# Optimization experiments

Measured on AMD Instinct MI355X. Metric: run time of the kernel, lower is better.

Reference implementation:

```python
import jax, jax.numpy as jnp
import numpy as np

B, H, C, HID, WIN, K = 8, 64, 128, 512, 4, 3
L = H * H

def _conv(x, w, groups, pad):
    return jax.lax.conv_general_dilated(
        x, w, (1, 1), [(pad, pad), (pad, pad)],
        dimension_numbers=('NCHW', 'OIHW', 'NCHW'), feature_group_count=groups)

def _ln(x, g, b):
    m = x.mean(-1, keepdims=True)
    v = ((x - m) ** 2).mean(-1, keepdims=True)
    return (x - m) * jax.lax.rsqrt(v + 1e-5) * g + b

def _gelu(x):
    return jax.nn.gelu(x, approximate=False)  # torch nn.GELU default = erf

def setup_inputs() -> dict:
    key = jax.random.key(0)
    ks = jax.random.split(key, 16)
    n = lambda i, sh: jax.random.normal(ks[i], sh, jnp.float32) * 0.02
    return dict(
        x=jax.random.normal(ks[0], (B, L, C), jnp.float32),
        ln1_g=jnp.ones((C,), jnp.float32), ln1_b=jnp.zeros((C,), jnp.float32),
        conv1_w=n(1, (WIN * C, C, K, K)),
        w_down=n(2, (WIN, C)), b_down=jnp.zeros((WIN,), jnp.float32),
        w1=n(3, (4 * WIN, WIN)), b1=jnp.zeros((4 * WIN,), jnp.float32),
        w2=n(4, (WIN, 4 * WIN)), b2=jnp.zeros((WIN,), jnp.float32),
        w_gk=n(5, (C, WIN * C)), b_gk=jnp.zeros((C,), jnp.float32),
        w_fus=n(6, (C, (WIN + 1) * C)), b_fus=jnp.zeros((C,), jnp.float32),
        ln2_g=jnp.ones((C,), jnp.float32), ln2_b=jnp.zeros((C,), jnp.float32),
        lin1_w=n(7, (HID, C)), lin1_b=jnp.zeros((HID,), jnp.float32),
        dw_w=n(8, (HID, 1, K, K)), dw_b=jnp.zeros((HID,), jnp.float32),
        lin2_w=n(9, (C, HID)), lin2_b=jnp.zeros((C,), jnp.float32),
    )

def _kernel_attn(x, conv1_w, w_down, b_down, w1, b1, w2, b2, w_gk, b_gk, w_fus, b_fus):
    ws = H // 2  # window grid is 2x2 since win_num=4
    xw = x.reshape(B, 2, ws, 2, ws, C).transpose(0, 1, 3, 5, 2, 4).reshape(B, WIN * C, ws, ws)
    wc = _conv(xw, conv1_w, WIN, 1)
    # WinKernel_Reweight (SE over windows)
    pooled = wc.mean((2, 3)).reshape(B, WIN, C)
    y = jnp.einsum('bgc,gc->bg', pooled, w_down) + b_down
    y = _gelu(y @ w1.T + b1)
    wgt = jax.nn.sigmoid(y @ w2.T + b2)
    k0 = conv1_w.reshape(WIN, C, C, K, K)
    kern = wgt[:, :, None, None, None, None] * k0[None]
    k_in = kern.transpose(0, 2, 1, 3, 4, 5).reshape(B * C, WIN * C, K, K)
    gk = jnp.einsum('om,nmij->noij', w_gk, k_in) + b_gk[None, :, None, None]
    kernels = jnp.concatenate([kern, gk.reshape(B, 1, C, C, K, K)], axis=1)
    kernels = kernels.reshape(B * (WIN + 1) * C, C, K, K)
    # per-sample dynamic grouped conv over full-resolution image
    ximg = x.reshape(B, H, H, C).transpose(0, 3, 1, 2)     # [B, C, H, W]
    xrep = jnp.tile(ximg, (1, WIN + 1, 1, 1)).reshape(1, B * (WIN + 1) * C, H, H)
    out = _conv(xrep, kernels, B * (WIN + 1), 1).reshape(B, (WIN + 1) * C, H, H)
    out = jnp.einsum('oc,bchw->bohw', w_fus, out) + b_fus[None, :, None, None]
    return out.transpose(0, 2, 3, 1).reshape(B, L, C)

def _leff(x, lin1_w, lin1_b, dw_w, dw_b, lin2_w, lin2_b):
    h = _gelu(x @ lin1_w.T + lin1_b)                       # [B, L, HID]
    h = h.reshape(B, H, H, HID).transpose(0, 3, 1, 2)
    h = _gelu(_conv(h, dw_w, HID, 1) + dw_b[None, :, None, None])  # depthwise 3x3
    h = h.transpose(0, 2, 3, 1).reshape(B, L, HID)
    return h @ lin2_w.T + lin2_b

def reference(x, ln1_g, ln1_b, conv1_w, w_down, b_down, w1, b1, w2, b2,
              w_gk, b_gk, w_fus, b_fus, ln2_g, ln2_b,
              lin1_w, lin1_b, dw_w, dw_b, lin2_w, lin2_b):
    x = x + _kernel_attn(_ln(x, ln1_g, ln1_b), conv1_w, w_down, b_down,
                         w1, b1, w2, b2, w_gk, b_gk, w_fus, b_fus)
    x = x + _leff(_ln(x, ln2_g, ln2_b), lin1_w, lin1_b, dw_w, dw_b, lin2_w, lin2_b)
    return x
```

## Files before the change

### kernel.cpp

```cpp
#include <hip/hip_runtime.h>
#include <math.h>

#define NB   8
#define HH   64
#define NC   128
#define NHID 512
#define NL   4096

typedef __attribute__((ext_vector_type(4))) float f32x4;
typedef __attribute__((ext_vector_type(8))) __bf16 bf16x8;

__device__ __forceinline__ float gelu_f(float v) {
  return 0.5f * v * (1.f + erff(v * 0.70710678118654752f));
}
__device__ __forceinline__ float sigmoid_f(float v) {
  return 1.f / (1.f + expf(-v));
}
__device__ __forceinline__ unsigned short f2bf(float f) {
  unsigned int u = __builtin_bit_cast(unsigned int, f);
  unsigned int r = (u + 0x7FFFu + ((u >> 16) & 1u)) >> 16;
  return (unsigned short)r;
}
__device__ __forceinline__ float bf2f(unsigned short h) {
  return __builtin_bit_cast(float, ((unsigned int)h) << 16);
}
__device__ __forceinline__ float bflo(unsigned int w) {
  return __builtin_bit_cast(float, w << 16);
}
__device__ __forceinline__ float bfhi(unsigned int w) {
  return __builtin_bit_cast(float, w & 0xFFFF0000u);
}
__device__ __forceinline__ void gld16(const void* g, void* l) {
  __builtin_amdgcn_global_load_lds(
      (const __attribute__((address_space(1))) unsigned int*)g,
      (__attribute__((address_space(3))) unsigned int*)l, 16, 0, 0);
}

__device__ __forceinline__ void bf16x8_store(const float4& a, const float4& b, void* dst) {
  unsigned int p0 = (unsigned int)f2bf(a.x) | ((unsigned int)f2bf(a.y) << 16);
  unsigned int p1 = (unsigned int)f2bf(a.z) | ((unsigned int)f2bf(a.w) << 16);
  unsigned int p2 = (unsigned int)f2bf(b.x) | ((unsigned int)f2bf(b.y) << 16);
  unsigned int p3 = (unsigned int)f2bf(b.z) | ((unsigned int)f2bf(b.w) << 16);
  *(uint4*)dst = make_uint4(p0, p1, p2, p3);
}

__global__ __launch_bounds__(256) void head_kernel(const float* __restrict__ x,
    const float* __restrict__ ln1_g, const float* __restrict__ ln1_b,
    unsigned short* __restrict__ xln,
    const float* __restrict__ lin1_w, const float* __restrict__ lin2_w,
    const float* __restrict__ w_gk, const float* __restrict__ w_fus,
    const float* __restrict__ dw_w, const float* __restrict__ conv1_w,
    unsigned short* __restrict__ w1o, unsigned short* __restrict__ w2o,
    unsigned short* __restrict__ wgko, unsigned short* __restrict__ wf1o,
    unsigned short* __restrict__ wf2o, float* __restrict__ dwt,
    float* __restrict__ sfus,
    unsigned short* __restrict__ ctp, unsigned short* __restrict__ ctq) {
  int gblk = blockIdx.x, tid = threadIdx.x;
  if (gblk < 8192) {
    int wv = tid >> 6, l = tid & 63;
    int row = gblk * 4 + wv;
    const float2 v = *(const float2*)(x + (size_t)row * NC + l * 2);
    float s = v.x + v.y, ss = v.x * v.x + v.y * v.y;
#pragma unroll
    for (int off = 32; off > 0; off >>= 1) {
      s  += __shfl_down(s, off);
      ss += __shfl_down(ss, off);
    }
    s = __shfl(s, 0); ss = __shfl(ss, 0);
    float mean = s * (1.f / NC);
    float rstd = rsqrtf(ss * (1.f / NC) - mean * mean + 1e-5f);
    const float2 gg = *(const float2*)(ln1_g + l * 2);
    const float2 bv = *(const float2*)(ln1_b + l * 2);
    float o0 = (v.x - mean) * rstd * gg.x + bv.x;
    float o1 = (v.y - mean) * rstd * gg.y + bv.y;
    unsigned int pk = (unsigned int)f2bf(o0) | ((unsigned int)f2bf(o1) << 16);
    *(unsigned int*)((char*)xln + (size_t)row * 256 + ((l >> 2) << 4) + (l & 3) * 4) = pk;
    return;
  }
  if (gblk < 8347) {
    int blk = gblk - 8192;
    if (blk < 32) {
      int idx = blk * 256 + tid;
      int n = idx >> 4, c16 = idx & 15;
      const float4 a = *(const float4*)(lin1_w + (size_t)n * 128 + c16 * 8);
      const float4 b = *(const float4*)(lin1_w + (size_t)n * 128 + c16 * 8 + 4);
      bf16x8_store(a, b, (char*)w1o + (size_t)n * 256 + ((c16 ^ (n & 7)) << 4));
    } else if (blk < 64) {
      int idx = (blk - 32) * 256 + tid;
      int kt = idx >> 11, c = (idx >> 4) & 127, c16 = idx & 15;
      const float* s = lin2_w + (size_t)c * NHID + kt * 128 + c16 * 8;
      const float4 a = *(const float4*)(s);
      const float4 b = *(const float4*)(s + 4);
      bf16x8_store(a, b, (char*)w2o + (size_t)(kt * 128 + c) * 256 + ((c16 ^ (c & 7)) << 4));
    } else if (blk < 96) {
      int idx = (blk - 64) * 256 + tid;
      int row = idx >> 4, c16 = idx & 15;
      int w = row >> 7, q = row & 127;
      const float* s = w_gk + (size_t)q * 512 + w * 128 + c16 * 8;
      const float4 a = *(const float4*)(s);
      const float4 b = *(const float4*)(s + 4);
      bf16x8_store(a, b, (char*)wgko + (size_t)row * 256 + ((c16 ^ (row & 7)) << 4));
    } else if (blk < 136) {
      int idx = (blk - 96) * 256 + tid;
      if (idx < 8192) {
        int row = idx >> 4, c16 = idx & 15;
        int w = row >> 7, o = row & 127;
        const float* s = w_fus + (size_t)o * 640 + w * 128 + c16 * 8;
        const float4 a = *(const float4*)(s);
        const float4 b = *(const float4*)(s + 4);
        bf16x8_store(a, b, (char*)wf1o + (size_t)row * 256 + ((c16 ^ (row & 7)) << 4));
      } else if (idx < 10240) {
        int i2 = idx - 8192;
        int row = i2 >> 4, c16 = i2 & 15;
        const float* s = w_fus + (size_t)row * 640 + 512 + c16 * 8;
        const float4 a = *(const float4*)(s);
        const float4 b = *(const float4*)(s + 4);
        bf16x8_store(a, b, (char*)wf2o + (size_t)row * 256 + ((c16 ^ (row & 7)) << 4));
      }
    } else if (blk < 154) {
      int idx = (blk - 136) * 256 + tid;
      if (idx < 4608) {
        int p = idx / 1152, rem = idx - p * 1152;
        int tap = rem >> 7, c = rem & 127;
        dwt[idx] = dw_w[(size_t)(p * 128 + c) * 9 + tap];
      }
    } else {
      if (tid < 128) {
        float s = 0;
        for (int p = 0; p < 128; ++p) s += w_fus[(size_t)tid * 640 + 512 + p];
        sfus[tid] = s;
      }
    }
    return;
  }
  {
    int oc = (gblk - 8347) * 2 + (tid >> 7);
    int w = oc >> 7, c = oc & 127;
    int t = tid & 127;
    float v[9];
#pragma unroll
    for (int j = 0; j < 9; ++j) v[j] = conv1_w[(size_t)oc * 1152 + t * 9 + j];
#pragma unroll
    for (int j = 0; j < 9; ++j) {
      unsigned short bv = f2bf(v[j]);
      size_t prow = (size_t)(w * 9 + j) * 128 + c;
      *(unsigned short*)((char*)ctp + prow * 256 + ((((t >> 3) ^ (c & 7)) << 4) + (t & 7) * 2)) = bv;
      size_t qrow = (size_t)(w * 9 + j) * 128 + t;
      *(unsigned short*)((char*)ctq + qrow * 256 + ((((c >> 3) ^ (t & 7)) << 4) + (c & 7) * 2)) = bv;
    }
  }
}

__global__ __launch_bounds__(128) void rs_kernel(const unsigned short* __restrict__ xln,
    float* __restrict__ RS) {
  int blk = blockIdx.x;
  int r = blk & 31, bw = blk >> 5;
  int win = bw & 3, b = bw >> 2;
  int hw = win >> 1, wn = win & 1;
  int cin = threadIdx.x;
  const unsigned short* base = xln + (((size_t)(b * 64 + hw * 32 + r)) * 64 + wn * 32) * NC + cin;
  float s = 0;
#pragma unroll
  for (int c = 0; c < 32; ++c) s += bf2f(base[(size_t)c * NC]);
  RS[(size_t)blk * 128 + cin] = s;
}

__global__ __launch_bounds__(256) void gemmGT_kernel(const unsigned short* __restrict__ Wgk,
    const unsigned short* __restrict__ CTP, const float* __restrict__ w_down,
    unsigned short* __restrict__ Gbf, float* __restrict__ U,
    const unsigned short* __restrict__ xln, const float* __restrict__ RS,
    float* __restrict__ T) {
  int gblk = blockIdx.x;
  int tid = threadIdx.x;
  if (gblk >= 36) {
    if (tid >= 128) return;
    int bw = gblk - 36;
    int win = bw & 3, b = bw >> 2;
    int hw = win >> 1, wn = win & 1;
    int cin = tid;
    const unsigned short* base = xln + (((size_t)(b * 64 + hw * 32)) * 64 + wn * 32) * NC + cin;
    float A = 0;
#pragma unroll
    for (int r = 0; r < 32; ++r) A += RS[(size_t)(bw * 32 + r) * 128 + cin];
    float r0  = RS[(size_t)(bw * 32) * 128 + cin];
    float r31 = RS[(size_t)(bw * 32 + 31) * 128 + cin];
    float c0 = 0, c31 = 0;
#pragma unroll
    for (int r = 0; r < 32; ++r) {
      c0  += bf2f(base[((size_t)r * 64) * NC]);
      c31 += bf2f(base[((size_t)r * 64 + 31) * NC]);
    }
    float x00 = bf2f(base[0]);
    float x0c = bf2f(base[(size_t)31 * NC]);
    float xr0 = bf2f(base[((size_t)31 * 64) * NC]);
    float xrc = bf2f(base[((size_t)31 * 64 + 31) * NC]);
    float* t = T + ((size_t)bw * 128 + cin) * 9;
    t[0] = A - r31 - c31 + xrc;
    t[1] = A - r31;
    t[2] = A - r31 - c0 + xr0;
    t[3] = A - c31;
    t[4] = A;
    t[5] = A - c0;
    t[6] = A - r0 - c31 + x0c;
    t[7] = A - r0;
    t[8] = A - r0 - c0 + x00;
    return;
  }
  __shared__ uint4 LA[2048];
  __shared__ uint4 LB[2048];
  int bx = gblk;
  int w = bx / 9;
  int wv = tid >> 6, l = tid & 63;
  const char* ga = (const char*)Wgk + (size_t)w * 32768;
  const char* gb = (const char*)CTP + (size_t)bx * 32768;
  for (int i = wv; i < 32; i += 4) gld16(ga + (i << 10) + l * 16, (char*)LA + (i << 10));
  for (int i = wv; i < 32; i += 4) gld16(gb + (i << 10) + l * 16, (char*)LB + (i << 10));
  __syncthreads();
  const f32x4 zero = {0.f, 0.f, 0.f, 0.f};
  f32x4 acc[2][8];
#pragma unroll
  for (int mt = 0; mt < 2; ++mt)
#pragma unroll
    for (int nt = 0; nt < 8; ++nt) acc[mt][nt] = zero;
  bf16x8 af[2][4];
#pragma unroll
  for (int mt = 0; mt < 2; ++mt) {
    int r = wv * 16 + mt * 64 + (l & 15);
#pragma unroll
    for (int ks = 0; ks < 4; ++ks) {
      int c16 = ks * 4 + (l >> 4);
      af[mt][ks] = *(const bf16x8*)((const char*)LA + r * 256 + ((c16 ^ (r & 7)) << 4));
    }
  }
#pragma unroll
  for (int nt = 0; nt < 8; ++nt) {
    int n = nt * 16 + (l & 15);
    bf16x8 bq[4];
#pragma unroll
    for (int ks = 0; ks < 4; ++ks) {
      int c16 = ks * 4 + (l >> 4);
      bq[ks] = *(const bf16x8*)((const char*)LB + n * 256 + ((c16 ^ (n & 7)) << 4));
    }
#pragma unroll
    for (int ks = 0; ks < 4; ++ks)
#pragma unroll
      for (int mt = 0; mt < 2; ++mt)
        acc[mt][nt] = __builtin_amdgcn_mfma_f32_16x16x32_bf16(af[mt][ks], bq[ks], acc[mt][nt], 0, 0, 0);
  }
  char* gout = (char*)Gbf + (size_t)bx * 32768;
#pragma unroll
  for (int mt = 0; mt < 2; ++mt)
#pragma unroll
    for (int nt = 0; nt < 8; ++nt) {
      int p = nt * 16 + (l & 15);
#pragma unroll
      for (int r2 = 0; r2 < 4; ++r2) {
        int q = wv * 16 + mt * 64 + (l >> 4) * 4 + r2;
        *(unsigned short*)(gout + q * 256 + ((((p >> 3) ^ (q & 7)) << 4) + (p & 7) * 2)) =
            f2bf(acc[mt][nt][r2]);
      }
    }
  if (tid < 128) {
    int cin = tid;
    int hi = cin >> 3, lo = (cin & 7) * 2;
    float s = 0;
    for (int cout = 0; cout < 128; ++cout) {
      unsigned short bv = *(const unsigned short*)((const char*)LB + cout * 256 +
                                                   (((hi ^ (cout & 7)) << 4) + lo));
      s += w_down[w * 128 + cout] * bf2f(bv);
    }
    U[(size_t)bx * 128 + cin] = s;
  }
}

__global__ __launch_bounds__(256) void gemmAWse_kernel(const unsigned short* __restrict__ Wf1,
    const unsigned short* __restrict__ CTQ, const unsigned short* __restrict__ Wf2,
    const unsigned short* __restrict__ Gbf, float* __restrict__ AW,
    const float* __restrict__ T, const float* __restrict__ U,
    const float* __restrict__ b_down, const float* __restrict__ w1,
    const float* __restrict__ b1, const float* __restrict__ w2,
    const float* __restrict__ b2, float* __restrict__ wgt) {
  __shared__ uint4 LA[2048];
  __shared__ uint4 LB[2048];
  int gblk = blockIdx.x;
  int tid = threadIdx.x;
  if (gblk == 36) {
    float* ydot = (float*)LA;
    int pair = tid >> 3, sub = tid & 7;
    int g = pair & 3;
    float acc = 0;
    for (int k = 0; k < 16; ++k) {
      int cin = sub * 16 + k;
      const float* tp = T + ((size_t)pair * 128 + cin) * 9;
#pragma unroll
      for (int ij = 0; ij < 9; ++ij)
        acc += U[(size_t)(g * 9 + ij) * 128 + cin] * tp[ij];
    }
#pragma unroll
    for (int off = 4; off > 0; off >>= 1) acc += __shfl_down(acc, off);
    if (sub == 0) ydot[pair] = acc;
    __syncthreads();
    if (tid < NB) {
      int b = tid;
      float y[4];
#pragma unroll
      for (int gg = 0; gg < 4; ++gg) y[gg] = ydot[b * 4 + gg] * (1.f / 1024.f) + b_down[gg];
      float y1[16];
#pragma unroll
      for (int i = 0; i < 16; ++i) {
        float a = b1[i];
#pragma unroll
        for (int gg = 0; gg < 4; ++gg) a += y[gg] * w1[i * 4 + gg];
        y1[i] = gelu_f(a);
      }
#pragma unroll
      for (int gg = 0; gg < 4; ++gg) {
        float a = b2[gg];
#pragma unroll
        for (int i = 0; i < 16; ++i) a += y1[i] * w2[gg * 16 + i];
        wgt[b * 4 + gg] = sigmoid_f(a);
      }
    }
    return;
  }
  int bx = gblk;
  int w = bx / 9;
  int wv = tid >> 6, l = tid & 63;
  const f32x4 zero = {0.f, 0.f, 0.f, 0.f};
  f32x4 acc[2][8];
#pragma unroll
  for (int mt = 0; mt < 2; ++mt)
#pragma unroll
    for (int nt = 0; nt < 8; ++nt) acc[mt][nt] = zero;
  for (int ph = 0; ph < 2; ++ph) {
    if (ph) __syncthreads();
    const char* ga = ph ? (const char*)Wf2 : (const char*)Wf1 + (size_t)w * 32768;
    const char* gb = ph ? (const char*)Gbf + (size_t)bx * 32768
                        : (const char*)CTQ + (size_t)bx * 32768;
    for (int i = wv; i < 32; i += 4) gld16(ga + (i << 10) + l * 16, (char*)LA + (i << 10));
    for (int i = wv; i < 32; i += 4) gld16(gb + (i << 10) + l * 16, (char*)LB + (i << 10));
    __syncthreads();
    bf16x8 af[2][4];
#pragma unroll
    for (int mt = 0; mt < 2; ++mt) {
      int r = wv * 16 + mt * 64 + (l & 15);
#pragma unroll
      for (int ks = 0; ks < 4; ++ks) {
        int c16 = ks * 4 + (l >> 4);
        af[mt][ks] = *(const bf16x8*)((const char*)LA + r * 256 + ((c16 ^ (r & 7)) << 4));
      }
    }
#pragma unroll
    for (int nt = 0; nt < 8; ++nt) {
      int n = nt * 16 + (l & 15);
      bf16x8 bq[4];
#pragma unroll
      for (int ks = 0; ks < 4; ++ks) {
        int c16 = ks * 4 + (l >> 4);
        bq[ks] = *(const bf16x8*)((const char*)LB + n * 256 + ((c16 ^ (n & 7)) << 4));
      }
#pragma unroll
      for (int ks = 0; ks < 4; ++ks)
#pragma unroll
        for (int mt = 0; mt < 2; ++mt)
          acc[mt][nt] = __builtin_amdgcn_mfma_f32_16x16x32_bf16(af[mt][ks], bq[ks], acc[mt][nt], 0, 0, 0);
    }
  }
  float* aout = AW + (size_t)bx * 16384;
#pragma unroll
  for (int mt = 0; mt < 2; ++mt)
#pragma unroll
    for (int nt = 0; nt < 8; ++nt) {
      int q = nt * 16 + (l & 15);
#pragma unroll
      for (int r2 = 0; r2 < 4; ++r2) {
        int o = wv * 16 + mt * 64 + (l >> 4) * 4 + r2;
        aout[(size_t)o * 128 + q] = acc[mt][nt][r2];
      }
    }
}

__global__ __launch_bounds__(128) void m_kernel(const float* __restrict__ AW,
    const float* __restrict__ wgt, const float* __restrict__ sfus,
    const float* __restrict__ b_gk, unsigned short* __restrict__ Mb) {
  int blk = blockIdx.x;
  int b = blk >> 7;
  int o = blk & 127;
  int q = threadIdx.x;
  float a3 = sfus[o] * b_gk[q];
  float acc[9];
#pragma unroll
  for (int ij = 0; ij < 9; ++ij) acc[ij] = a3;
#pragma unroll
  for (int w = 0; w < 4; ++w) {
    float wv = wgt[b * 4 + w];
#pragma unroll
    for (int ij = 0; ij < 9; ++ij)
      acc[ij] += wv * AW[(((size_t)(w * 9 + ij) * 128 + o) * 128) + q];
  }
  int qswz = (q & 7) | (((q >> 3) ^ (o & 7)) << 3);
#pragma unroll
  for (int ij = 0; ij < 9; ++ij)
    Mb[(((size_t)(b * 9 + ij) * NC + o) * NC) + qswz] = f2bf(acc[ij]);
}

__global__ __launch_bounds__(256) void conv_kernel(const float* __restrict__ x0,
    const unsigned short* __restrict__ xln, const unsigned short* __restrict__ Mb,
    const float* __restrict__ b_fus, const float* __restrict__ ln2g,
    const float* __restrict__ ln2b, float* __restrict__ xout,
    unsigned short* __restrict__ xln2) {
  __shared__ uint4 XT[1600];
  __shared__ uint4 MT[2048];
  int bx = blockIdx.x;
  int b = bx >> 6, tile = bx & 63;
  int by = (tile >> 3) * 8, bxc = (tile & 7) * 8;
  int tid = threadIdx.x, wv = tid >> 6, l = tid & 63;
  for (int i = tid; i < 1600; i += 256) {
    int cell = i >> 4, c16 = i & 15;
    int pr = cell / 10, pc = cell - pr * 10;
    int gy = by + pr - 1, gx = bxc + pc - 1;
    uint4 v = make_uint4(0, 0, 0, 0);
    if ((unsigned)gy < 64u && (unsigned)gx < 64u)
      v = *(const uint4*)(xln + (((size_t)b * NL + gy * 64 + gx) * NC + c16 * 8));
    *(uint4*)((char*)XT + cell * 256 + ((c16 ^ (cell & 7)) << 4)) = v;
  }
  const char* mg = (const char*)Mb + (size_t)b * 9 * 32768;
  for (int i = wv; i < 32; i += 4) gld16(mg + (i << 10) + l * 16, (char*)MT + (i << 10));
  __syncthreads();

  const f32x4 zero = {0.f, 0.f, 0.f, 0.f};
  f32x4 acc[8];
#pragma unroll
  for (int nt = 0; nt < 8; ++nt) acc[nt] = zero;

  int sp = wv * 16 + (l & 15);
  int srow = sp >> 3, scol = sp & 7;

  for (int ij = 0; ij < 9; ++ij) {
    int di = ij / 3, dj = ij - di * 3;
    int cell = (srow + di) * 10 + scol + dj;
    bf16x8 af[4];
#pragma unroll
    for (int ks = 0; ks < 4; ++ks) {
      int c16 = ks * 4 + (l >> 4);
      af[ks] = *(const bf16x8*)((const char*)XT + cell * 256 + ((c16 ^ (cell & 7)) << 4));
    }
#pragma unroll
    for (int nt = 0; nt < 8; ++nt) {
      int oc = nt * 16 + (l & 15);
      bf16x8 bq[4];
#pragma unroll
      for (int ks = 0; ks < 4; ++ks) {
        int c16 = ks * 4 + (l >> 4);
        bq[ks] = *(const bf16x8*)((const char*)MT + oc * 256 + ((c16 ^ (oc & 7)) << 4));
      }
#pragma unroll
      for (int ks = 0; ks < 4; ++ks)
        acc[nt] = __builtin_amdgcn_mfma_f32_16x16x32_bf16(af[ks], bq[ks], acc[nt], 0, 0, 0);
    }
    __syncthreads();
    if (ij < 8) {
      const char* mg2 = mg + (size_t)(ij + 1) * 32768;
      for (int i = wv; i < 32; i += 4) gld16(mg2 + (i << 10) + l * 16, (char*)MT + (i << 10));
    }
    __syncthreads();
  }
  float s[4] = {0, 0, 0, 0}, ss2[4] = {0, 0, 0, 0};
  float vals[8][4];
#pragma unroll
  for (int nt = 0; nt < 8; ++nt) {
    int oc = nt * 16 + (l & 15);
    float bfv = b_fus[oc];
#pragma unroll
    for (int r2 = 0; r2 < 4; ++r2) {
      int sp2 = wv * 16 + (l >> 4) * 4 + r2;
      int gy = by + (sp2 >> 3), gx = bxc + (sp2 & 7);
      size_t gi = ((size_t)b * NL + gy * 64 + gx) * NC + oc;
      float v = x0[gi] + acc[nt][r2] + bfv;
      xout[gi] = v;
      vals[nt][r2] = v;
      s[r2] += v;
      ss2[r2] += v * v;
    }
  }
#pragma unroll
  for (int r2 = 0; r2 < 4; ++r2) {
#pragma unroll
    for (int off = 1; off < 16; off <<= 1) {
      s[r2]   += __shfl_xor(s[r2], off);
      ss2[r2] += __shfl_xor(ss2[r2], off);
    }
  }
  float mean[4], rstd[4];
#pragma unroll
  for (int r2 = 0; r2 < 4; ++r2) {
    mean[r2] = s[r2] * (1.f / 128.f);
    rstd[r2] = rsqrtf(ss2[r2] * (1.f / 128.f) - mean[r2] * mean[r2] + 1e-5f);
  }
#pragma unroll
  for (int nt = 0; nt < 8; ++nt) {
    int oc = nt * 16 + (l & 15);
    float gv = ln2g[oc], bv = ln2b[oc];
    int cc16 = oc >> 3, cby = (oc & 7) * 2;
#pragma unroll
    for (int r2 = 0; r2 < 4; ++r2) {
      int sp2 = wv * 16 + (l >> 4) * 4 + r2;
      int gy = by + (sp2 >> 3), gx = bxc + (sp2 & 7);
      size_t rowg = (size_t)b * NL + gy * 64 + gx;
      float o = (vals[nt][r2] - mean[r2]) * rstd[r2] * gv + bv;
      *(unsigned short*)((char*)xln2 + rowg * 256 + (((size_t)(cc16 ^ (int)(rowg & 7))) << 4) + cby) = f2bf(o);
    }
  }
}

__global__ __launch_bounds__(256) void lin1_kernel(const unsigned short* __restrict__ xa,
    const unsigned short* __restrict__ wb, const float* __restrict__ bias,
    unsigned short* __restrict__ h1p0, unsigned short* __restrict__ h1p123) {
  __shared__ uint4 XA[1024];
  __shared__ uint4 XB[2048];
  size_t rb = (size_t)blockIdx.x * 64;
  int tid = threadIdx.x, wv = tid >> 6, l = tid & 63;
  const char* ga = (const char*)xa + rb * 256;
  for (int i = wv; i < 16; i += 4) gld16(ga + (i << 10) + l * 16, (char*)XA + (i << 10));
  for (int i = wv; i < 32; i += 4) gld16((const char*)wb + (i << 10) + l * 16, (char*)XB + (i << 10));
  __syncthreads();
  int r = wv * 16 + (l & 15);
  bf16x8 af[4];
#pragma unroll
  for (int ks = 0; ks < 4; ++ks) {
    int c16 = ks * 4 + (l >> 4);
    af[ks] = *(const bf16x8*)((const char*)XA + r * 256 + ((c16 ^ (r & 7)) << 4));
  }
  const f32x4 zero = {0.f, 0.f, 0.f, 0.f};
  for (int cb = 0; cb < 4; ++cb) {
    f32x4 acc[8];
#pragma unroll
    for (int nt = 0; nt < 8; ++nt) acc[nt] = zero;
#pragma unroll
    for (int nt = 0; nt < 8; ++nt) {
      int n = nt * 16 + (l & 15);
      bf16x8 bq[4];
#pragma unroll
      for (int ks = 0; ks < 4; ++ks) {
        int c16 = ks * 4 + (l >> 4);
        bq[ks] = *(const bf16x8*)((const char*)XB + n * 256 + ((c16 ^ (n & 7)) << 4));
      }
#pragma unroll
      for (int ks = 0; ks < 4; ++ks)
        acc[nt] = __builtin_amdgcn_mfma_f32_16x16x32_bf16(af[ks], bq[ks], acc[nt], 0, 0, 0);
    }
    if (cb < 3) {
      __syncthreads();
      const char* gb = (const char*)wb + (size_t)(cb + 1) * 32768;
      for (int i = wv; i < 32; i += 4) gld16(gb + (i << 10) + l * 16, (char*)XB + (i << 10));
    }
    unsigned short* hp = (cb == 0) ? h1p0 : h1p123 + (size_t)(cb - 1) * 4194304;
#pragma unroll
    for (int nt = 0; nt < 8; ++nt) {
      int n = nt * 16 + (l & 15);
      float bsv = bias[cb * 128 + n];
#pragma unroll
      for (int r2 = 0; r2 < 4; ++r2) {
        size_t row = rb + wv * 16 + (l >> 4) * 4 + r2;
        hp[row * 128 + n] = f2bf(gelu_f(acc[nt][r2] + bsv));
      }
    }
    if (cb < 3) __syncthreads();
  }
}

__global__ __launch_bounds__(256) void dw_kernel(const unsigned short* __restrict__ h1p0,
    const unsigned short* __restrict__ h1p123, const float* __restrict__ dwt,
    const float* __restrict__ dw_b, unsigned short* __restrict__ h2p0,
    unsigned short* __restrict__ h2p123) {
  __shared__ unsigned char HT[6 * 64 * 128];
  __shared__ float wsm[9][64];
  int bx = blockIdx.x;
  int cp = bx >> 7;
  int rem = bx & 127;
  int bimg = rem >> 4, ys = rem & 15;
  int p = cp >> 1, chh = cp & 1;
  int y0 = ys * 4;
  int tid = threadIdx.x, wv = tid >> 6, l = tid & 63;
  const unsigned short* h1p = p ? h1p123 + (size_t)(p - 1) * 4194304 : h1p0;
  unsigned short* h2p = p ? h2p123 + (size_t)(p - 1) * 4194304 : h2p0;
  size_t ibase = (size_t)bimg * 4096;
  for (int i = tid; i < 576; i += 256)
    wsm[0][i] = dwt[(size_t)p * 1152 + (i >> 6) * 128 + chh * 64 + (i & 63)];
#pragma unroll
  for (int it = 0; it < 12; ++it) {
    int cb = it * 4 + wv;
    int row = cb >> 3, colblk = cb & 7;
    int yy = y0 - 1 + row;
    int ldsbase = (row * 64 + colblk * 8) * 128;
    if ((unsigned)yy < 64u) {
      const char* src = (const char*)h1p +
          (ibase + (size_t)yy * 64 + colblk * 8 + (l >> 3)) * 256 + chh * 128 + (l & 7) * 16;
      gld16(src, (char*)HT + ldsbase);
    } else {
      *(uint4*)((char*)HT + ldsbase + l * 16) = make_uint4(0, 0, 0, 0);
    }
  }
  int grp = tid >> 3, c8 = tid & 7;
  int ch0 = p * 128 + chh * 64 + c8 * 8;
  const float4 bs0 = *(const float4*)(dw_b + ch0);
  const float4 bs1 = *(const float4*)(dw_b + ch0 + 4);
  __syncthreads();

#pragma unroll
  for (int r = 0; r < 4; ++r) {
#pragma unroll
    for (int cc = 0; cc < 2; ++cc) {
      int col = grp * 2 + cc;
      float acw[8];
      acw[0] = bs0.x; acw[1] = bs0.y; acw[2] = bs0.z; acw[3] = bs0.w;
      acw[4] = bs1.x; acw[5] = bs1.y; acw[6] = bs1.z; acw[7] = bs1.w;
#pragma unroll
      for (int dy = 0; dy < 3; ++dy) {
#pragma unroll
        for (int dx = 0; dx < 3; ++dx) {
          int xc = col + dx - 1;
          if ((unsigned)xc < 64u) {
            const uint4 u = *(const uint4*)((const char*)HT +
                (((r + dy) * 64 + xc) * 128) + c8 * 16);
            const float4 wa  = *(const float4*)(&wsm[dy * 3 + dx][c8 * 8]);
            const float4 wb2 = *(const float4*)(&wsm[dy * 3 + dx][c8 * 8 + 4]);
            acw[0] += wa.x * bflo(u.x);  acw[1] += wa.y * bfhi(u.x);
            acw[2] += wa.z * bflo(u.y);  acw[3] += wa.w * bfhi(u.y);
            acw[4] += wb2.x * bflo(u.z); acw[5] += wb2.y * bfhi(u.z);
            acw[6] += wb2.z * bflo(u.w); acw[7] += wb2.w * bfhi(u.w);
          }
        }
      }
      size_t sidx = ibase + (size_t)(y0 + r) * 64 + col;
      int c16o = chh * 8 + c8;
      unsigned int o0 = (unsigned int)f2bf(gelu_f(acw[0])) | ((unsigned int)f2bf(gelu_f(acw[1])) << 16);
      unsigned int o1 = (unsigned int)f2bf(gelu_f(acw[2])) | ((unsigned int)f2bf(gelu_f(acw[3])) << 16);
      unsigned int o2 = (unsigned int)f2bf(gelu_f(acw[4])) | ((unsigned int)f2bf(gelu_f(acw[5])) << 16);
      unsigned int o3 = (unsigned int)f2bf(gelu_f(acw[6])) | ((unsigned int)f2bf(gelu_f(acw[7])) << 16);
      *(uint4*)(h2p + sidx * 128 + ((c16o ^ (int)(sidx & 7)) << 3)) = make_uint4(o0, o1, o2, o3);
    }
  }
}

__global__ __launch_bounds__(256) void lin2_kernel(const unsigned short* __restrict__ h2p0,
    const unsigned short* __restrict__ h2p123, const unsigned short* __restrict__ wb,
    const float* __restrict__ bias, const float* __restrict__ xres, float* __restrict__ out) {
  __shared__ uint4 XA[1024];
  __shared__ uint4 XB[2048];
  size_t rb = (size_t)blockIdx.x * 64;
  int tid = threadIdx.x, wv = tid >> 6, l = tid & 63;
  const f32x4 zero = {0.f, 0.f, 0.f, 0.f};
  f32x4 acc[8];
#pragma unroll
  for (int nt = 0; nt < 8; ++nt) acc[nt] = zero;
  int r = wv * 16 + (l & 15);
  for (int kt = 0; kt < 4; ++kt) {
    if (kt) __syncthreads();
    const unsigned short* hp = (kt == 0) ? h2p0 : h2p123 + (size_t)(kt - 1) * 4194304;
    const char* ga = (const char*)hp + rb * 256;
    const char* gb = (const char*)wb + (size_t)kt * 32768;
    for (int i = wv; i < 16; i += 4) gld16(ga + (i << 10) + l * 16, (char*)XA + (i << 10));
    for (int i = wv; i < 32; i += 4) gld16(gb + (i << 10) + l * 16, (char*)XB + (i << 10));
    __syncthreads();
    bf16x8 af[4];
#pragma unroll
    for (int ks = 0; ks < 4; ++ks) {
      int c16 = ks * 4 + (l >> 4);
      af[ks] = *(const bf16x8*)((const char*)XA + r * 256 + ((c16 ^ (r & 7)) << 4));
    }
#pragma unroll
    for (int nt = 0; nt < 8; ++nt) {
      int n = nt * 16 + (l & 15);
      bf16x8 bq[4];
#pragma unroll
      for (int ks = 0; ks < 4; ++ks) {
        int c16 = ks * 4 + (l >> 4);
        bq[ks] = *(const bf16x8*)((const char*)XB + n * 256 + ((c16 ^ (n & 7)) << 4));
      }
#pragma unroll
      for (int ks = 0; ks < 4; ++ks)
        acc[nt] = __builtin_amdgcn_mfma_f32_16x16x32_bf16(af[ks], bq[ks], acc[nt], 0, 0, 0);
    }
  }
#pragma unroll
  for (int nt = 0; nt < 8; ++nt) {
    int n = nt * 16 + (l & 15);
    float bsv = bias[n];
#pragma unroll
    for (int r2 = 0; r2 < 4; ++r2) {
      size_t row = rb + wv * 16 + (l >> 4) * 4 + r2;
      size_t gi = row * NC + n;
      out[gi] = xres[gi] + acc[nt][r2] + bsv;
    }
  }
}

extern "C" void kernel_launch(void* const* d_in, const int* in_sizes, int n_in,
                              void* d_out, int out_size, void* d_ws, size_t ws_size,
                              hipStream_t stream) {
  (void)in_sizes; (void)n_in; (void)out_size; (void)ws_size;
  const float* x       = (const float*)d_in[0];
  const float* ln1_g   = (const float*)d_in[1];
  const float* ln1_b   = (const float*)d_in[2];
  const float* conv1_w = (const float*)d_in[3];
  const float* w_down  = (const float*)d_in[4];
  const float* b_down  = (const float*)d_in[5];
  const float* w1      = (const float*)d_in[6];
  const float* b1      = (const float*)d_in[7];
  const float* w2      = (const float*)d_in[8];
  const float* b2      = (const float*)d_in[9];
  const float* w_gk    = (const float*)d_in[10];
  const float* b_gk    = (const float*)d_in[11];
  const float* w_fus   = (const float*)d_in[12];
  const float* b_fus   = (const float*)d_in[13];
  const float* ln2_g   = (const float*)d_in[14];
  const float* ln2_b   = (const float*)d_in[15];
  const float* lin1_w  = (const float*)d_in[16];
  const float* lin1_b  = (const float*)d_in[17];
  const float* dw_w    = (const float*)d_in[18];
  const float* dw_b    = (const float*)d_in[19];
  const float* lin2_w  = (const float*)d_in[20];
  const float* lin2_b  = (const float*)d_in[21];
  float* out = (float*)d_out;
  char* ws = (char*)d_ws;

  float*          xatt    = (float*)(ws);
  float*          Tb      = (float*)(ws + 16777216);
  float*          wgtb    = (float*)(ws + 16924672);
  float*          sfus    = (float*)(ws + 16925184);
  float*          dwt     = (float*)(ws + 16925696);
  unsigned short* Wgk_bf  = (unsigned short*)(ws + 16944128);
  unsigned short* Wf1_bf  = (unsigned short*)(ws + 17075200);
  unsigned short* Wf2_bf  = (unsigned short*)(ws + 17206272);
  unsigned short* w1_bf   = (unsigned short*)(ws + 17239040);
  unsigned short* w2_bf   = (unsigned short*)(ws + 17370112);
  unsigned short* M_bf    = (unsigned short*)(ws + 17501184);
  unsigned short* xln_bf  = (unsigned short*)(ws + 19860480);
  unsigned short* xln2_bf = (unsigned short*)(ws + 28249088);
  unsigned short* h1p123  = (unsigned short*)(ws + 36637696);
  unsigned short* h2p123  = (unsigned short*)(ws + 61803520);
  char* sc = ws + 28249088;
  float*          RSb     = (float*)(sc);
  float*          Ub      = (float*)(sc + 524288);
  unsigned short* CTP_bf  = (unsigned short*)(sc + 542720);
  unsigned short* CTQ_bf  = (unsigned short*)(sc + 1722368);
  unsigned short* G_bf    = (unsigned short*)(sc + 2902016);
  float*          AWb     = (float*)(sc + 4081664);

  head_kernel<<<8603, 256, 0, stream>>>(x, ln1_g, ln1_b, xln_bf,
                                        lin1_w, lin2_w, w_gk, w_fus, dw_w, conv1_w,
                                        w1_bf, w2_bf, Wgk_bf, Wf1_bf, Wf2_bf, dwt, sfus,
                                        CTP_bf, CTQ_bf);
  rs_kernel<<<1024, 128, 0, stream>>>(xln_bf, RSb);
  gemmGT_kernel<<<68, 256, 0, stream>>>(Wgk_bf, CTP_bf, w_down, G_bf, Ub,
                                        xln_bf, RSb, Tb);
  gemmAWse_kernel<<<37, 256, 0, stream>>>(Wf1_bf, CTQ_bf, Wf2_bf, G_bf, AWb,
                                          Tb, Ub, b_down, w1, b1, w2, b2, wgtb);
  m_kernel<<<1024, 128, 0, stream>>>(AWb, wgtb, sfus, b_gk, M_bf);
  conv_kernel<<<512, 256, 0, stream>>>(x, xln_bf, M_bf, b_fus, ln2_g, ln2_b, xatt, xln2_bf);
  lin1_kernel<<<512, 256, 0, stream>>>(xln2_bf, w1_bf, lin1_b, xln_bf , h1p123);
  dw_kernel<<<1024, 256, 0, stream>>>(xln_bf , h1p123, dwt, dw_b,
                                      xln2_bf , h2p123);
  lin2_kernel<<<512, 256, 0, stream>>>(xln2_bf , h2p123, w2_bf, lin2_b, xatt, out);
}
```

Measured before the change: 150.8 us.

## Double-buffer conv weight tiles in halves and store residual intermediate as bf16

```diff
diff --git a/kernel.cpp b/kernel.cpp
--- a/kernel.cpp
+++ b/kernel.cpp
@@ -407,10 +407,10 @@
 __global__ __launch_bounds__(256) void conv_kernel(const float* __restrict__ x0,
     const unsigned short* __restrict__ xln, const unsigned short* __restrict__ Mb,
     const float* __restrict__ b_fus, const float* __restrict__ ln2g,
-    const float* __restrict__ ln2b, float* __restrict__ xout,
+    const float* __restrict__ ln2b, unsigned short* __restrict__ xatt,
     unsigned short* __restrict__ xln2) {
   __shared__ uint4 XT[1600];
-  __shared__ uint4 MT[2048];
+  __shared__ uint4 MT[2][1024];
   int bx = blockIdx.x;
   int b = bx >> 6, tile = bx & 63;
   int by = (tile >> 3) * 8, bxc = (tile & 7) * 8;
@@ -425,7 +425,7 @@
     *(uint4*)((char*)XT + cell * 256 + ((c16 ^ (cell & 7)) << 4)) = v;
   }
   const char* mg = (const char*)Mb + (size_t)b * 9 * 32768;
-  for (int i = wv; i < 32; i += 4) gld16(mg + (i << 10) + l * 16, (char*)MT + (i << 10));
+  for (int i = wv; i < 16; i += 4) gld16(mg + (i << 10) + l * 16, (char*)MT[0] + (i << 10));
   __syncthreads();
 
   const f32x4 zero = {0.f, 0.f, 0.f, 0.f};
@@ -435,35 +435,40 @@
 
   int sp = wv * 16 + (l & 15);
   int srow = sp >> 3, scol = sp & 7;
-
-  for (int ij = 0; ij < 9; ++ij) {
-    int di = ij / 3, dj = ij - di * 3;
-    int cell = (srow + di) * 10 + scol + dj;
-    bf16x8 af[4];
-#pragma unroll
-    for (int ks = 0; ks < 4; ++ks) {
-      int c16 = ks * 4 + (l >> 4);
-      af[ks] = *(const bf16x8*)((const char*)XT + cell * 256 + ((c16 ^ (cell & 7)) << 4));
-    }
-#pragma unroll
-    for (int nt = 0; nt < 8; ++nt) {
-      int oc = nt * 16 + (l & 15);
-      bf16x8 bq[4];
+  int buf = 0;
+  bf16x8 af[4];
+
+  for (int p = 0; p < 18; ++p) {
+    int ij = p >> 1, h = p & 1;
+    if (p < 17) {
+      const char* src = mg + (size_t)(p + 1) * 16384;
+      for (int i = wv; i < 16; i += 4) gld16(src + (i << 10) + l * 16, (char*)MT[buf ^ 1] + (i << 10));
+    }
+    if (h == 0) {
+      int di = ij / 3, dj = ij - di * 3;
+      int cell = (srow + di) * 10 + scol + dj;
 #pragma unroll
       for (int ks = 0; ks < 4; ++ks) {
         int c16 = ks * 4 + (l >> 4);
-        bq[ks] = *(const bf16x8*)((const char*)MT + oc * 256 + ((c16 ^ (oc & 7)) << 4));
+        af[ks] = *(const bf16x8*)((const char*)XT + cell * 256 + ((c16 ^ (cell & 7)) << 4));
+      }
+    }
+#pragma unroll
+    for (int nt4 = 0; nt4 < 4; ++nt4) {
+      int nt = h * 4 + nt4;
+      int ocl = nt4 * 16 + (l & 15);
+      bf16x8 bq[4];
+#pragma unroll
+      for (int ks = 0; ks < 4; ++ks) {
+        int c16 = ks * 4 + (l >> 4);
+        bq[ks] = *(const bf16x8*)((const char*)MT[buf] + ocl * 256 + ((c16 ^ (ocl & 7)) << 4));
       }
 #pragma unroll
       for (int ks = 0; ks < 4; ++ks)
         acc[nt] = __builtin_amdgcn_mfma_f32_16x16x32_bf16(af[ks], bq[ks], acc[nt], 0, 0, 0);
     }
     __syncthreads();
-    if (ij < 8) {
-      const char* mg2 = mg + (size_t)(ij + 1) * 32768;
-      for (int i = wv; i < 32; i += 4) gld16(mg2 + (i << 10) + l * 16, (char*)MT + (i << 10));
-    }
-    __syncthreads();
+    buf ^= 1;
   }
   float s[4] = {0, 0, 0, 0}, ss2[4] = {0, 0, 0, 0};
   float vals[8][4];
@@ -477,7 +482,7 @@
       int gy = by + (sp2 >> 3), gx = bxc + (sp2 & 7);
       size_t gi = ((size_t)b * NL + gy * 64 + gx) * NC + oc;
       float v = x0[gi] + acc[nt][r2] + bfv;
-      xout[gi] = v;
+      xatt[gi] = f2bf(v);
       vals[nt][r2] = v;
       s[r2] += v;
       ss2[r2] += v * v;
@@ -645,7 +650,8 @@
 
 __global__ __launch_bounds__(256) void lin2_kernel(const unsigned short* __restrict__ h2p0,
     const unsigned short* __restrict__ h2p123, const unsigned short* __restrict__ wb,
-    const float* __restrict__ bias, const float* __restrict__ xres, float* __restrict__ out) {
+    const float* __restrict__ bias, const unsigned short* __restrict__ xres,
+    float* __restrict__ out) {
   __shared__ uint4 XA[1024];
   __shared__ uint4 XB[2048];
   size_t rb = (size_t)blockIdx.x * 64;
@@ -691,7 +697,7 @@
     for (int r2 = 0; r2 < 4; ++r2) {
       size_t row = rb + wv * 16 + (l >> 4) * 4 + r2;
       size_t gi = row * NC + n;
-      out[gi] = xres[gi] + acc[nt][r2] + bsv;
+      out[gi] = bf2f(xres[gi]) + acc[nt][r2] + bsv;
     }
   }
 }
@@ -725,7 +731,7 @@
   float* out = (float*)d_out;
   char* ws = (char*)d_ws;
 
-  float*          xatt    = (float*)(ws);
+  unsigned short* xatt_bf = (unsigned short*)(ws);
   float*          Tb      = (float*)(ws + 16777216);
   float*          wgtb    = (float*)(ws + 16924672);
   float*          sfus    = (float*)(ws + 16925184);
@@ -758,9 +764,9 @@
   gemmAWse_kernel<<<37, 256, 0, stream>>>(Wf1_bf, CTQ_bf, Wf2_bf, G_bf, AWb,
                                           Tb, Ub, b_down, w1, b1, w2, b2, wgtb);
   m_kernel<<<1024, 128, 0, stream>>>(AWb, wgtb, sfus, b_gk, M_bf);
-  conv_kernel<<<512, 256, 0, stream>>>(x, xln_bf, M_bf, b_fus, ln2_g, ln2_b, xatt, xln2_bf);
+  conv_kernel<<<512, 256, 0, stream>>>(x, xln_bf, M_bf, b_fus, ln2_g, ln2_b, xatt_bf, xln2_bf);
   lin1_kernel<<<512, 256, 0, stream>>>(xln2_bf, w1_bf, lin1_b, xln_bf , h1p123);
   dw_kernel<<<1024, 256, 0, stream>>>(xln_bf , h1p123, dwt, dw_b,
                                       xln2_bf , h2p123);
-  lin2_kernel<<<512, 256, 0, stream>>>(xln2_bf , h2p123, w2_bf, lin2_b, xatt, out);
-}
+  lin2_kernel<<<512, 256, 0, stream>>>(xln2_bf , h2p123, w2_bf, lin2_b, xatt_bf, out);
+}
```

Result: slower. 165.8 us (+10.0%).
